# Performance work log

Measured on AMD Instinct MI355X. Metric: run time of the kernel, lower is better.

Reference implementation:

```python
import jax, jax.numpy as jnp
import numpy as np

NEG_FILL = -1e4  # finite stand-in for -inf so sort/cumsum stay NaN-free


def entmax15(X):
    """1.5-entmax along the last axis (Peters et al. 2019, sort-based exact algorithm)."""
    X = X - jnp.max(X, axis=-1, keepdims=True)
    X = X * 0.5  # alpha=1.5 transform
    Xsrt = -jnp.sort(-X, axis=-1)  # descending sort
    S = X.shape[-1]
    rho = jnp.arange(1, S + 1, dtype=X.dtype)  # 1..S support-size candidates
    mean = jnp.cumsum(Xsrt, axis=-1) / rho
    mean_sq = jnp.cumsum(Xsrt * Xsrt, axis=-1) / rho
    ss = rho * (mean_sq - mean * mean)          # running k*variance
    delta = (1.0 - ss) / rho
    tau = mean - jnp.sqrt(jnp.clip(delta, 0.0, None))
    support_size = jnp.sum(tau <= Xsrt, axis=-1, keepdims=True)
    tau_star = jnp.take_along_axis(tau, support_size - 1, axis=-1)
    return jnp.square(jnp.clip(X - tau_star, 0.0, None))


def setup_inputs() -> dict:
    key = jax.random.key(0)
    k1, k2 = jax.random.split(key)
    B, S = 32768, 2048
    scores = jax.random.normal(k1, (B, S), dtype=jnp.float32)
    mask = jax.random.randint(k2, (B, S), 0, 2, dtype=jnp.int32)
    mask = mask.at[:, 0].set(1)  # guarantee at least one unmasked token per row
    return {"scores": scores, "mask": mask}


def reference(scores, mask):
    # replace_masked_values(scores, mask, -inf) -> entmax15(dim=-1)
    masked_scores = jnp.where(mask.astype(bool), scores, NEG_FILL)
    return entmax15(masked_scores)
```

## Files before the change

kernel.cpp:

```cpp
#include <hip/hip_runtime.h>


#define NEG_FILL (-1.0e4f)

static constexpr int S_DIM = 2048;
static constexpr int WAVES_PER_BLOCK = 4;
static constexpr int ELEMS = S_DIM / 64;
static constexpr int VEC = ELEMS / 4;

__global__ __launch_bounds__(256) void entmax15_kernel(
    const float* __restrict__ scores,
    const int*   __restrict__ mask,
    float*       __restrict__ out,
    int nrows)
{
    const int lane = threadIdx.x & 63;
    const int wave = threadIdx.x >> 6;
    const int row  = blockIdx.x * WAVES_PER_BLOCK + wave;
    if (row >= nrows) return;

    const size_t base = (size_t)row * S_DIM;
    const float4* __restrict__ srow = (const float4*)(scores + base);
    const int4*   __restrict__ mrow = (const int4*)(mask + base);
    float4*       __restrict__ orow = (float4*)(out + base);

    float x[ELEMS];
    float rmax = -3.402823466e38f;
#pragma unroll
    for (int j = 0; j < VEC; ++j) {
        const float4 s = srow[lane + 64 * j];
        const int4   m = mrow[lane + 64 * j];
        float v0 = m.x ? s.x : NEG_FILL;
        float v1 = m.y ? s.y : NEG_FILL;
        float v2 = m.z ? s.z : NEG_FILL;
        float v3 = m.w ? s.w : NEG_FILL;
        x[4 * j + 0] = v0;
        x[4 * j + 1] = v1;
        x[4 * j + 2] = v2;
        x[4 * j + 3] = v3;
        rmax = fmaxf(rmax, fmaxf(fmaxf(v0, v1), fmaxf(v2, v3)));
    }
#pragma unroll
    for (int off = 32; off >= 1; off >>= 1)
        rmax = fmaxf(rmax, __shfl_xor(rmax, off, 64));

    const float shift = -0.5f * rmax;
#pragma unroll
    for (int i = 0; i < ELEMS; ++i)
        x[i] = fmaf(0.5f, x[i], shift);

    float tau = -1.0f;
#pragma unroll 1
    for (int it = 0; it < 16; ++it) {
        float F = 0.0f, G = 0.0f, K = 0.0f;
#pragma unroll
        for (int i = 0; i < ELEMS; ++i) {
            float d = x[i] - tau;
            float y = fmaxf(d, 0.0f);
            F = fmaf(y, y, F);
            G += y;
            K += (d > 0.0f) ? 1.0f : 0.0f;
        }
#pragma unroll
        for (int off = 32; off >= 1; off >>= 1) {
            F += __shfl_xor(F, off, 64);
            G += __shfl_xor(G, off, 64);
            K += __shfl_xor(K, off, 64);
        }
        const float c = F - 1.0f;
        const float disc = fmaf(G, G, -K * c);
        const float denom = (disc > 0.0f) ? (G + sqrtf(disc)) : (2.0f * G);
        const float u = c / denom;
        tau += u;
        if (!(fabsf(u) > 2e-7f)) break;
    }

#pragma unroll
    for (int j = 0; j < VEC; ++j) {
        float y0 = fmaxf(x[4 * j + 0] - tau, 0.0f);
        float y1 = fmaxf(x[4 * j + 1] - tau, 0.0f);
        float y2 = fmaxf(x[4 * j + 2] - tau, 0.0f);
        float y3 = fmaxf(x[4 * j + 3] - tau, 0.0f);
        float4 o;
        o.x = y0 * y0;
        o.y = y1 * y1;
        o.z = y2 * y2;
        o.w = y3 * y3;
        orow[lane + 64 * j] = o;
    }
}

extern "C" void kernel_launch(void* const* d_in, const int* in_sizes, int n_in,
                              void* d_out, int out_size, void* d_ws, size_t ws_size,
                              hipStream_t stream) {
    const float* scores = (const float*)d_in[0];
    const int*   mask   = (const int*)d_in[1];
    float*       out    = (float*)d_out;

    const int nrows = in_sizes[0] / S_DIM;
    const int grid  = (nrows + WAVES_PER_BLOCK - 1) / WAVES_PER_BLOCK;

    entmax15_kernel<<<grid, 256, 0, stream>>>(scores, mask, out, nrows);
}
```

Before: 586.4 us.

## Process two rows per wave with packed float2 math and ballot-based counts

```diff
diff --git a/kernel.cpp b/kernel.cpp
--- a/kernel.cpp
+++ b/kernel.cpp
@@ -2,11 +2,15 @@
 
 
 #define NEG_FILL (-1.0e4f)
+
+typedef float float2v __attribute__((ext_vector_type(2)));
 
 static constexpr int S_DIM = 2048;
 static constexpr int WAVES_PER_BLOCK = 4;
+static constexpr int ROWS_PER_WAVE = 2;
 static constexpr int ELEMS = S_DIM / 64;
 static constexpr int VEC = ELEMS / 4;
+static constexpr int VEC2 = ELEMS / 2;
 
 __global__ __launch_bounds__(256) void entmax15_kernel(
     const float* __restrict__ scores,
@@ -16,77 +20,171 @@
 {
     const int lane = threadIdx.x & 63;
     const int wave = threadIdx.x >> 6;
-    const int row  = blockIdx.x * WAVES_PER_BLOCK + wave;
-    if (row >= nrows) return;
-
-    const size_t base = (size_t)row * S_DIM;
-    const float4* __restrict__ srow = (const float4*)(scores + base);
-    const int4*   __restrict__ mrow = (const int4*)(mask + base);
-    float4*       __restrict__ orow = (float4*)(out + base);
-
-    float x[ELEMS];
-    float rmax = -3.402823466e38f;
+    const int rowA = (blockIdx.x * WAVES_PER_BLOCK + wave) * ROWS_PER_WAVE;
+    if (rowA >= nrows) return;
+    const bool hasB = (rowA + 1) < nrows;
+    const int rowB = hasB ? (rowA + 1) : rowA;
+
+    const size_t baseA = (size_t)rowA * S_DIM;
+    const size_t baseB = (size_t)rowB * S_DIM;
+    const float4* __restrict__ srowA = (const float4*)(scores + baseA);
+    const int4*   __restrict__ mrowA = (const int4*)(mask + baseA);
+    float4*       __restrict__ orowA = (float4*)(out + baseA);
+    const float4* __restrict__ srowB = (const float4*)(scores + baseB);
+    const int4*   __restrict__ mrowB = (const int4*)(mask + baseB);
+    float4*       __restrict__ orowB = (float4*)(out + baseB);
+
+    float xA[ELEMS], xB[ELEMS];
+    float rmaxA = -3.402823466e38f, rmaxB = -3.402823466e38f;
 #pragma unroll
     for (int j = 0; j < VEC; ++j) {
-        const float4 s = srow[lane + 64 * j];
-        const int4   m = mrow[lane + 64 * j];
-        float v0 = m.x ? s.x : NEG_FILL;
-        float v1 = m.y ? s.y : NEG_FILL;
-        float v2 = m.z ? s.z : NEG_FILL;
-        float v3 = m.w ? s.w : NEG_FILL;
-        x[4 * j + 0] = v0;
-        x[4 * j + 1] = v1;
-        x[4 * j + 2] = v2;
-        x[4 * j + 3] = v3;
-        rmax = fmaxf(rmax, fmaxf(fmaxf(v0, v1), fmaxf(v2, v3)));
-    }
-#pragma unroll
-    for (int off = 32; off >= 1; off >>= 1)
-        rmax = fmaxf(rmax, __shfl_xor(rmax, off, 64));
-
-    const float shift = -0.5f * rmax;
-#pragma unroll
-    for (int i = 0; i < ELEMS; ++i)
-        x[i] = fmaf(0.5f, x[i], shift);
-
-    float tau = -1.0f;
+        const float4 sa = srowA[lane + 64 * j];
+        const int4   ma = mrowA[lane + 64 * j];
+        const float4 sb = srowB[lane + 64 * j];
+        const int4   mb = mrowB[lane + 64 * j];
+        float a0 = ma.x ? sa.x : NEG_FILL;
+        float a1 = ma.y ? sa.y : NEG_FILL;
+        float a2 = ma.z ? sa.z : NEG_FILL;
+        float a3 = ma.w ? sa.w : NEG_FILL;
+        float b0 = mb.x ? sb.x : NEG_FILL;
+        float b1 = mb.y ? sb.y : NEG_FILL;
+        float b2 = mb.z ? sb.z : NEG_FILL;
+        float b3 = mb.w ? sb.w : NEG_FILL;
+        xA[4 * j + 0] = a0; xA[4 * j + 1] = a1; xA[4 * j + 2] = a2; xA[4 * j + 3] = a3;
+        xB[4 * j + 0] = b0; xB[4 * j + 1] = b1; xB[4 * j + 2] = b2; xB[4 * j + 3] = b3;
+        rmaxA = fmaxf(rmaxA, fmaxf(fmaxf(a0, a1), fmaxf(a2, a3)));
+        rmaxB = fmaxf(rmaxB, fmaxf(fmaxf(b0, b1), fmaxf(b2, b3)));
+    }
+#pragma unroll
+    for (int off = 32; off >= 1; off >>= 1) {
+        rmaxA = fmaxf(rmaxA, __shfl_xor(rmaxA, off, 64));
+        rmaxB = fmaxf(rmaxB, __shfl_xor(rmaxB, off, 64));
+    }
+
+    const float2v h05   = {0.5f, 0.5f};
+    const float2v one2  = {1.0f, 1.0f};
+    const float2v zero2 = {0.0f, 0.0f};
+    const float2v shA = {-0.5f * rmaxA, -0.5f * rmaxA};
+    const float2v shB = {-0.5f * rmaxB, -0.5f * rmaxB};
+    float2v* xvA = (float2v*)xA;
+    float2v* xvB = (float2v*)xB;
+
+    float2v FA = zero2, GA = zero2, FB = zero2, GB = zero2;
+    int KA = 0, KB = 0;
+#pragma unroll
+    for (int i = 0; i < VEC2; ++i) {
+        float2v ta = __builtin_elementwise_fma(xvA[i], h05, shA);
+        float2v tb = __builtin_elementwise_fma(xvB[i], h05, shB);
+        xvA[i] = ta;
+        xvB[i] = tb;
+        float2v da = ta + one2;
+        float2v db = tb + one2;
+        float2v ya = __builtin_elementwise_max(da, zero2);
+        float2v yb = __builtin_elementwise_max(db, zero2);
+        FA = __builtin_elementwise_fma(ya, ya, FA);
+        FB = __builtin_elementwise_fma(yb, yb, FB);
+        GA = GA + ya;
+        GB = GB + yb;
+        KA += __popcll(__ballot(da.x > 0.0f));
+        KA += __popcll(__ballot(da.y > 0.0f));
+        KB += __popcll(__ballot(db.x > 0.0f));
+        KB += __popcll(__ballot(db.y > 0.0f));
+    }
+
+    float2v RA, RB;
+    RA.x = FA.x + FA.y; RA.y = GA.x + GA.y;
+    RB.x = FB.x + FB.y; RB.y = GB.x + GB.y;
+#pragma unroll
+    for (int off = 32; off >= 1; off >>= 1) {
+        float2v ta, tb;
+        ta.x = __shfl_xor(RA.x, off, 64);
+        ta.y = __shfl_xor(RA.y, off, 64);
+        tb.x = __shfl_xor(RB.x, off, 64);
+        tb.y = __shfl_xor(RB.y, off, 64);
+        RA += ta;
+        RB += tb;
+    }
+
+    float cA     = RA.x - 1.0f;
+    float cB     = RB.x - 1.0f;
+    float discA  = fmaf(RA.y, RA.y, -(float)KA * cA);
+    float discB  = fmaf(RB.y, RB.y, -(float)KB * cB);
+    float denA   = (discA > 0.0f) ? (RA.y + sqrtf(discA)) : (2.0f * RA.y);
+    float denB   = (discB > 0.0f) ? (RB.y + sqrtf(discB)) : (2.0f * RB.y);
+    float uA     = cA / denA;
+    float uB     = cB / denB;
+    float tauA   = -1.0f + uA;
+    float tauB   = -1.0f + uB;
+
 #pragma unroll 1
-    for (int it = 0; it < 16; ++it) {
-        float F = 0.0f, G = 0.0f, K = 0.0f;
-#pragma unroll
-        for (int i = 0; i < ELEMS; ++i) {
-            float d = x[i] - tau;
-            float y = fmaxf(d, 0.0f);
-            F = fmaf(y, y, F);
-            G += y;
-            K += (d > 0.0f) ? 1.0f : 0.0f;
+    for (int it = 1; it < 16; ++it) {
+        if (!(fabsf(uA) > 2e-7f) && !(fabsf(uB) > 2e-7f)) break;
+        const float2v tA2 = {tauA, tauA};
+        const float2v tB2 = {tauB, tauB};
+        FA = zero2; GA = zero2; FB = zero2; GB = zero2;
+        KA = 0; KB = 0;
+#pragma unroll
+        for (int i = 0; i < VEC2; ++i) {
+            float2v da = xvA[i] - tA2;
+            float2v db = xvB[i] - tB2;
+            float2v ya = __builtin_elementwise_max(da, zero2);
+            float2v yb = __builtin_elementwise_max(db, zero2);
+            FA = __builtin_elementwise_fma(ya, ya, FA);
+            FB = __builtin_elementwise_fma(yb, yb, FB);
+            GA = GA + ya;
+            GB = GB + yb;
+            KA += __popcll(__ballot(da.x > 0.0f));
+            KA += __popcll(__ballot(da.y > 0.0f));
+            KB += __popcll(__ballot(db.x > 0.0f));
+            KB += __popcll(__ballot(db.y > 0.0f));
         }
+        RA.x = FA.x + FA.y; RA.y = GA.x + GA.y;
+        RB.x = FB.x + FB.y; RB.y = GB.x + GB.y;
 #pragma unroll
         for (int off = 32; off >= 1; off >>= 1) {
-            F += __shfl_xor(F, off, 64);
-            G += __shfl_xor(G, off, 64);
-            K += __shfl_xor(K, off, 64);
+            float2v ta, tb;
+            ta.x = __shfl_xor(RA.x, off, 64);
+            ta.y = __shfl_xor(RA.y, off, 64);
+            tb.x = __shfl_xor(RB.x, off, 64);
+            tb.y = __shfl_xor(RB.y, off, 64);
+            RA += ta;
+            RB += tb;
         }
-        const float c = F - 1.0f;
-        const float disc = fmaf(G, G, -K * c);
-        const float denom = (disc > 0.0f) ? (G + sqrtf(disc)) : (2.0f * G);
-        const float u = c / denom;
-        tau += u;
-        if (!(fabsf(u) > 2e-7f)) break;
-    }
-
+        cA    = RA.x - 1.0f;
+        cB    = RB.x - 1.0f;
+        discA = fmaf(RA.y, RA.y, -(float)KA * cA);
+        discB = fmaf(RB.y, RB.y, -(float)KB * cB);
+        denA  = (discA > 0.0f) ? (RA.y + sqrtf(discA)) : (2.0f * RA.y);
+        denB  = (discB > 0.0f) ? (RB.y + sqrtf(discB)) : (2.0f * RB.y);
+        uA    = cA / denA;
+        uB    = cB / denB;
+        tauA += uA;
+        tauB += uB;
+    }
+
+    const float2v tA2 = {tauA, tauA};
+    const float2v tB2 = {tauB, tauB};
 #pragma unroll
     for (int j = 0; j < VEC; ++j) {
-        float y0 = fmaxf(x[4 * j + 0] - tau, 0.0f);
-        float y1 = fmaxf(x[4 * j + 1] - tau, 0.0f);
-        float y2 = fmaxf(x[4 * j + 2] - tau, 0.0f);
-        float y3 = fmaxf(x[4 * j + 3] - tau, 0.0f);
-        float4 o;
-        o.x = y0 * y0;
-        o.y = y1 * y1;
-        o.z = y2 * y2;
-        o.w = y3 * y3;
-        orow[lane + 64 * j] = o;
+        float2v ya0 = __builtin_elementwise_max(xvA[2 * j]     - tA2, zero2);
+        float2v ya1 = __builtin_elementwise_max(xvA[2 * j + 1] - tA2, zero2);
+        float2v oa0 = ya0 * ya0;
+        float2v oa1 = ya1 * ya1;
+        float4 oa;
+        oa.x = oa0.x; oa.y = oa0.y; oa.z = oa1.x; oa.w = oa1.y;
+        orowA[lane + 64 * j] = oa;
+    }
+    if (hasB) {
+#pragma unroll
+        for (int j = 0; j < VEC; ++j) {
+            float2v yb0 = __builtin_elementwise_max(xvB[2 * j]     - tB2, zero2);
+            float2v yb1 = __builtin_elementwise_max(xvB[2 * j + 1] - tB2, zero2);
+            float2v ob0 = yb0 * yb0;
+            float2v ob1 = yb1 * yb1;
+            float4 ob;
+            ob.x = ob0.x; ob.y = ob0.y; ob.z = ob1.x; ob.w = ob1.y;
+            orowB[lane + 64 * j] = ob;
+        }
     }
 }
 
@@ -98,7 +196,8 @@
     float*       out    = (float*)d_out;
 
     const int nrows = in_sizes[0] / S_DIM;
-    const int grid  = (nrows + WAVES_PER_BLOCK - 1) / WAVES_PER_BLOCK;
+    const int rows_per_block = WAVES_PER_BLOCK * ROWS_PER_WAVE;
+    const int grid = (nrows + rows_per_block - 1) / rows_per_block;
 
     entmax15_kernel<<<grid, 256, 0, stream>>>(scores, mask, out, nrows);
 }
```

Measured after the change: 590.1 us. Within noise of the previous version (+0.6%).
